# Kernel optimization log

Measured on AMD Instinct MI355X. Metric: run time of the kernel, lower is better.

Reference implementation:

```python
import jax, jax.numpy as jnp
import numpy as np

N, DIM, DK, DV = 8192, 512, 128, 128


def setup_inputs() -> dict:
    key = jax.random.key(0)
    ks = jax.random.split(key, 6)
    s = lambda d: 1.0 / np.sqrt(d)
    return {
        "x": jax.random.normal(ks[0], (N, DIM), jnp.float32),
        "W": jax.random.normal(ks[1], (DK, DIM), jnp.float32) * s(DIM),
        "b": jax.random.normal(ks[2], (DK,), jnp.float32) * s(DIM),
        "Wv": jax.random.normal(ks[3], (DV, DIM), jnp.float32) * s(DIM),
        "bv": jax.random.normal(ks[4], (DV,), jnp.float32) * s(DIM),
        "a": jax.random.normal(ks[5], (2 * DK,), jnp.float32),
    }


def reference(x, W, b, Wv, bv, a):
    dk = a.shape[0] // 2
    wx = x @ W.T + b                      # [n, dk]
    # additive GAT score decomposed into two matvecs + outer sum
    s_src = wx @ a[:dk]                   # [n]
    s_dst = wx @ a[dk:]                   # [n]
    score = s_src[:, None] + s_dst[None, :]  # [n, n]
    score = jax.nn.leaky_relu(score, negative_slope=0.01)
    score = jax.nn.softmax(score, axis=-1)
    v = x @ Wv.T + bv                     # [n, dv]
    return score @ v                      # [n, dv]
```

## Files before the change

### kernel.cpp

```cpp
#include <hip/hip_runtime.h>
#include <math.h>

static constexpr int N    = 8192;
static constexpr int DIM  = 512;
static constexpr int DK   = 128;
static constexpr int DV   = 128;
static constexpr float SLOPE = 0.01f;

static constexpr int NCH  = 512;
static constexpr int CHSZ = 16;
static constexpr int NCOL = 258;

static constexpr int MT  = 128;
static constexpr int BK  = 32;
static constexpr int LDT = 132;

__global__ __launch_bounds__(256) void k_front(const float* __restrict__ x,
                                               const float* __restrict__ W,
                                               const float* __restrict__ b,
                                               const float* __restrict__ a,
                                               float* __restrict__ s_src,
                                               float* __restrict__ s_dst) {
    __shared__ float sa[2 * DK];
    __shared__ float sus[DIM + 32], sud[DIM + 32];
    __shared__ float sc[2];
    int tid = threadIdx.x;
    sa[tid] = a[tid];
    __syncthreads();

    {
        float p = 0.0f;
        if (tid < 64)        p = b[tid] * sa[tid] + b[tid + 64] * sa[tid + 64];
        else if (tid < 128) { int l = tid - 64; p = b[l] * sa[DK + l] + b[l + 64] * sa[DK + 64 + l]; }
#pragma unroll
        for (int off = 32; off > 0; off >>= 1) p += __shfl_down(p, off);
        if (tid == 0)  sc[0] = p;
        if (tid == 64) sc[1] = p;
    }

#pragma unroll
    for (int half = 0; half < 2; ++half) {
        int d = tid + half * 256;
        float us = 0.0f, ud = 0.0f;
#pragma unroll 4
        for (int k = 0; k < DK; ++k) {
            float w = W[(size_t)k * DIM + d];
            us += w * sa[k];
            ud += w * sa[DK + k];
        }
        int dp = d + (d >> 6) * 4;
        sus[dp] = us;
        sud[dp] = ud;
    }
    __syncthreads();

    int r   = tid >> 3;
    int seg = tid & 7;
    int row = blockIdx.x * 32 + r;
    const float* xr = x + (size_t)row * DIM;
    int base  = seg * 64;
    int baseP = base + seg * 4;
    float accs = 0.0f, accd = 0.0f;
#pragma unroll
    for (int i = 0; i < 16; ++i) {
        float4 q  = *reinterpret_cast<const float4*>(xr + base + i * 4);
        float4 u4 = *reinterpret_cast<const float4*>(&sus[baseP + i * 4]);
        float4 w4 = *reinterpret_cast<const float4*>(&sud[baseP + i * 4]);
        accs += q.x * u4.x + q.y * u4.y + q.z * u4.z + q.w * u4.w;
        accd += q.x * w4.x + q.y * w4.y + q.z * w4.z + q.w * w4.w;
    }
#pragma unroll
    for (int off = 4; off > 0; off >>= 1) {
        accs += __shfl_down(accs, off);
        accd += __shfl_down(accd, off);
    }
    if (seg == 0) {
        s_src[row] = accs + sc[0];
        s_dst[row] = accd + sc[1];
    }
}

__global__ __launch_bounds__(256) void k_v(const float* __restrict__ x,
                                           const float* __restrict__ Wv,
                                           float* __restrict__ vpart, int ksplit) {
    __shared__ float At[BK][LDT];
    __shared__ float Bt[BK][LDT];
    int tid = threadIdx.x;
    int mt  = blockIdx.x & 63;
    int ks  = blockIdx.x >> 6;
    int row0 = mt * MT;
    int ksub = DIM / ksplit;
    int kb0  = ks * ksub;
    int nt   = ksub / BK;
    int tx = tid & 15, ty = tid >> 4;

    float acc[8][8];
#pragma unroll
    for (int i = 0; i < 8; ++i)
#pragma unroll
        for (int j = 0; j < 8; ++j) acc[i][j] = 0.0f;

    int fr[4], fk[4];
#pragma unroll
    for (int i = 0; i < 4; ++i) {
        int f = tid + i * 256;
        fr[i] = f >> 3;
        fk[i] = (f & 7) * 4;
    }
    float4 px[4], pw[4];
#pragma unroll
    for (int i = 0; i < 4; ++i) {
        px[i] = *reinterpret_cast<const float4*>(x  + (size_t)(row0 + fr[i]) * DIM + kb0 + fk[i]);
        pw[i] = *reinterpret_cast<const float4*>(Wv + (size_t)fr[i] * DIM + kb0 + fk[i]);
    }

    for (int t = 0; t < nt; ++t) {
#pragma unroll
        for (int i = 0; i < 4; ++i) {
            At[fk[i] + 0][fr[i]] = px[i].x;
            At[fk[i] + 1][fr[i]] = px[i].y;
            At[fk[i] + 2][fr[i]] = px[i].z;
            At[fk[i] + 3][fr[i]] = px[i].w;
            Bt[fk[i] + 0][fr[i]] = pw[i].x;
            Bt[fk[i] + 1][fr[i]] = pw[i].y;
            Bt[fk[i] + 2][fr[i]] = pw[i].z;
            Bt[fk[i] + 3][fr[i]] = pw[i].w;
        }
        __syncthreads();
        if (t < nt - 1) {
            int kb = kb0 + (t + 1) * BK;
#pragma unroll
            for (int i = 0; i < 4; ++i) {
                px[i] = *reinterpret_cast<const float4*>(x  + (size_t)(row0 + fr[i]) * DIM + kb + fk[i]);
                pw[i] = *reinterpret_cast<const float4*>(Wv + (size_t)fr[i] * DIM + kb + fk[i]);
            }
        }
#pragma unroll 4
        for (int kk = 0; kk < BK; ++kk) {
            float4 a0 = *reinterpret_cast<const float4*>(&At[kk][ty * 4]);
            float4 a1 = *reinterpret_cast<const float4*>(&At[kk][64 + ty * 4]);
            float4 b0 = *reinterpret_cast<const float4*>(&Bt[kk][tx * 4]);
            float4 b1 = *reinterpret_cast<const float4*>(&Bt[kk][64 + tx * 4]);
            float av[8] = {a0.x, a0.y, a0.z, a0.w, a1.x, a1.y, a1.z, a1.w};
            float bw[8] = {b0.x, b0.y, b0.z, b0.w, b1.x, b1.y, b1.z, b1.w};
#pragma unroll
            for (int i = 0; i < 8; ++i)
#pragma unroll
                for (int j = 0; j < 8; ++j) acc[i][j] += av[i] * bw[j];
        }
        __syncthreads();
    }

#pragma unroll
    for (int rh = 0; rh < 2; ++rh)
#pragma unroll
        for (int i = 0; i < 4; ++i) {
            int row = row0 + rh * 64 + ty * 4 + i;
            float* dst = vpart + ((size_t)ks * N + row) * DV;
#pragma unroll
            for (int ch = 0; ch < 2; ++ch) {
                float4 o;
                o.x = acc[rh * 4 + i][ch * 4 + 0];
                o.y = acc[rh * 4 + i][ch * 4 + 1];
                o.z = acc[rh * 4 + i][ch * 4 + 2];
                o.w = acc[rh * 4 + i][ch * 4 + 3];
                *reinterpret_cast<float4*>(dst + ch * 64 + tx * 4) = o;
            }
        }
}

__global__ __launch_bounds__(256) void k_rank_scatter(const float* __restrict__ s_dst,
                                                      float* __restrict__ d_sorted,
                                                      int* __restrict__ perm) {
    __shared__ __align__(16) float sd[N];
    __shared__ int part[256];
    int tid = threadIdx.x;
    for (int t = tid; t < N / 4; t += 256)
        reinterpret_cast<float4*>(sd)[t] = reinterpret_cast<const float4*>(s_dst)[t];
    __syncthreads();
    int j0  = blockIdx.x * 16;
    int jj  = tid >> 4;
    int seg = tid & 15;
    int j   = j0 + jj;
    float dj = sd[j];
    int cnt = 0;
    const float4* sdv = reinterpret_cast<const float4*>(sd);
    int cbase = seg * 128;
    for (int c = 0; c < 128; ++c) {
        float4 q = sdv[cbase + c];
        int i0 = (cbase + c) * 4;
        cnt += (q.x < dj || (q.x == dj && (i0 + 0) < j));
        cnt += (q.y < dj || (q.y == dj && (i0 + 1) < j));
        cnt += (q.z < dj || (q.z == dj && (i0 + 2) < j));
        cnt += (q.w < dj || (q.w == dj && (i0 + 3) < j));
    }
    part[tid] = cnt;
    __syncthreads();
    if (tid < 16) {
        int s = 0;
#pragma unroll
        for (int t = 0; t < 16; ++t) s += part[tid * 16 + t];
        int jw = j0 + tid;
        d_sorted[s] = sd[jw];
        perm[s] = jw;
    }
}

__global__ __launch_bounds__(256) void k_vredY(const float* __restrict__ vpart,
                                               const float* __restrict__ bv,
                                               const float* __restrict__ d_sorted,
                                               const int* __restrict__ perm,
                                               float* __restrict__ Y1,
                                               float* __restrict__ Y2,
                                               double* __restrict__ chunk_tot,
                                               int ksplit) {
    __shared__ float sv[CHSZ][DV];
    __shared__ float se1[CHSZ], se2[CHSZ];
    int ch  = blockIdx.x;
    int tid = threadIdx.x;
    int g   = tid >> 5;
    int c4  = tid & 31;
    float dmax = d_sorted[N - 1];
    if (tid < CHSZ) {
        float d = d_sorted[ch * CHSZ + tid];
        se1[tid] = expf(d - dmax);
        se2[tid] = expf(SLOPE * d);
    }
    __syncthreads();
    float4 bb = reinterpret_cast<const float4*>(bv)[c4];
#pragma unroll
    for (int half = 0; half < 2; ++half) {
        int rl = half * 8 + g;
        int r  = ch * CHSZ + rl;
        int j  = perm[r];
        float4 s = {0.f, 0.f, 0.f, 0.f};
        for (int ksp = 0; ksp < ksplit; ++ksp) {
            float4 q = *reinterpret_cast<const float4*>(vpart + ((size_t)ksp * N + j) * DV + c4 * 4);
            s.x += q.x; s.y += q.y; s.z += q.z; s.w += q.w;
        }
        s.x += bb.x; s.y += bb.y; s.z += bb.z; s.w += bb.w;
        *reinterpret_cast<float4*>(&sv[rl][c4 * 4]) = s;
        float e1 = se1[rl], e2 = se2[rl];
        float4 o1 = {e1 * s.x, e1 * s.y, e1 * s.z, e1 * s.w};
        float4 o2 = {e2 * s.x, e2 * s.y, e2 * s.z, e2 * s.w};
        *reinterpret_cast<float4*>(Y1 + (size_t)r * DV + c4 * 4) = o1;
        *reinterpret_cast<float4*>(Y2 + (size_t)r * DV + c4 * 4) = o2;
    }
    __syncthreads();
    int col = tid & 127;
    bool is2 = tid >= 128;
    double acc = 0.0;
#pragma unroll
    for (int k = 0; k < CHSZ; ++k) {
        float e = is2 ? se2[k] : se1[k];
        acc += (double)(e * sv[k][col]);
    }
    chunk_tot[(size_t)ch * NCOL + tid] = acc;
    if (tid == 0) {
        double z = 0.0;
#pragma unroll
        for (int k = 0; k < CHSZ; ++k) z += (double)se1[k];
        chunk_tot[(size_t)ch * NCOL + 256] = z;
    }
    if (tid == 1) {
        double z = 0.0;
#pragma unroll
        for (int k = 0; k < CHSZ; ++k) z += (double)se2[k];
        chunk_tot[(size_t)ch * NCOL + 257] = z;
    }
}

__global__ __launch_bounds__(256) void k_coff(const double* __restrict__ chunk_tot,
                                              double* __restrict__ chunk_off,
                                              double* __restrict__ totals) {
    __shared__ double sp[256];
    int col = blockIdx.x;
    int tid = threadIdx.x;
    double v0 = chunk_tot[(size_t)(2 * tid) * NCOL + col];
    double v1 = chunk_tot[(size_t)(2 * tid + 1) * NCOL + col];
    double p = v0 + v1;
    sp[tid] = p;
    __syncthreads();
    for (int off = 1; off < 256; off <<= 1) {
        double t = (tid >= off) ? sp[tid - off] : 0.0;
        __syncthreads();
        sp[tid] += t;
        __syncthreads();
    }
    double excl = sp[tid] - p;
    chunk_off[(size_t)(2 * tid) * NCOL + col]     = excl;
    chunk_off[(size_t)(2 * tid + 1) * NCOL + col] = excl + v0;
    if (tid == 255) totals[col] = sp[255];
}

__global__ __launch_bounds__(256) void k_scanW(const float* __restrict__ Y1,
                                               const float* __restrict__ Y2,
                                               const float* __restrict__ d_sorted,
                                               const double* __restrict__ chunk_off,
                                               float* __restrict__ P1,
                                               float* __restrict__ P2,
                                               double* __restrict__ pz1,
                                               double* __restrict__ pz2) {
    int ch  = blockIdx.x;
    int tid = threadIdx.x;
    int col = tid & 127;
    bool is2 = tid >= 128;
    const float* Y = is2 ? Y2 : Y1;
    float* P       = is2 ? P2 : P1;
    double acc = chunk_off[(size_t)ch * NCOL + tid];
#pragma unroll
    for (int k = 0; k < CHSZ; ++k) {
        size_t idx = (size_t)(ch * CHSZ + k) * DV + col;
        P[idx] = (float)acc;
        acc += (double)Y[idx];
    }
    if (tid < 2) {
        float dmax = d_sorted[N - 1];
        double z = chunk_off[(size_t)ch * NCOL + 256 + tid];
        double* pz = tid == 0 ? pz1 : pz2;
#pragma unroll
        for (int k = 0; k < CHSZ; ++k) {
            int r = ch * CHSZ + k;
            float d = d_sorted[r];
            float e = (tid == 0) ? expf(d - dmax) : expf(SLOPE * d);
            pz[r] = z;
            z += (double)e;
        }
    }
}

__global__ __launch_bounds__(256) void k_final(const float* __restrict__ s_src,
                                               const float* __restrict__ d_sorted,
                                               const float* __restrict__ P1,
                                               const float* __restrict__ P2,
                                               const double* __restrict__ pz1,
                                               const double* __restrict__ pz2,
                                               const double* __restrict__ totals,
                                               float* __restrict__ out) {
    __shared__ int ski[8];
    __shared__ float ssi[8];
    int tid = threadIdx.x;
    int rbase = blockIdx.x * 8;
    if (tid < 8) {
        int row = rbase + tid;
        float si = s_src[row];
        float thr = -si;
        int lo = 0, hi = N;
        while (lo < hi) {
            int mid = (lo + hi) >> 1;
            if (d_sorted[mid] <= thr) lo = mid + 1; else hi = mid;
        }
        ski[tid] = lo;
        ssi[tid] = si;
    }
    __syncthreads();
    float dmax = d_sorted[N - 1];
    int dv = tid & 127;
    int half = tid >> 7;
    double T1 = totals[dv];
    double T2 = totals[128 + dv];
    double z1T = totals[256], z2T = totals[257];
#pragma unroll
    for (int it = 0; it < 4; ++it) {
        int r2 = it * 2 + half;
        int row = rbase + r2;
        float si = ssi[r2];
        int ki = ski[r2];
        float t = si + dmax;
        float m = t > 0.0f ? t : SLOPE * t;
        float alpha = expf(t - m);
        float beta  = expf(SLOPE * si - m);
        double suf1, sufz1, pre2, prez2;
        if (ki < N) {
            suf1  = T1 - (double)P1[(size_t)ki * DV + dv];
            sufz1 = z1T - pz1[ki];
            pre2  = (double)P2[(size_t)ki * DV + dv];
            prez2 = pz2[ki];
        } else {
            suf1 = 0.0; sufz1 = 0.0; pre2 = T2; prez2 = z2T;
        }
        double num = (double)alpha * suf1  + (double)beta * pre2;
        double den = (double)alpha * sufz1 + (double)beta * prez2;
        out[(size_t)row * DV + dv] = (float)(num / den);
    }
}

extern "C" void kernel_launch(void* const* d_in, const int* in_sizes, int n_in,
                              void* d_out, int out_size, void* d_ws, size_t ws_size,
                              hipStream_t stream) {
    const float* x  = (const float*)d_in[0];
    const float* W  = (const float*)d_in[1];
    const float* b  = (const float*)d_in[2];
    const float* Wv = (const float*)d_in[3];
    const float* bv = (const float*)d_in[4];
    const float* a  = (const float*)d_in[5];
    float* out = (float*)d_out;

    char* base = (char*)d_ws;
    size_t off = 0;
    auto carve = [&](size_t bytes) -> void* {
        void* p = base + off;
        off = (off + bytes + 255) & ~(size_t)255;
        return p;
    };
    float*  s_src     = (float*)carve(N * sizeof(float));
    float*  s_dst     = (float*)carve(N * sizeof(float));
    float*  d_sorted  = (float*)carve(N * sizeof(float));
    int*    perm      = (int*)carve(N * sizeof(int));
    double* pz1       = (double*)carve(N * sizeof(double));
    double* pz2       = (double*)carve(N * sizeof(double));
    double* chunk_tot = (double*)carve((size_t)NCH * NCOL * sizeof(double));
    double* chunk_off = (double*)carve((size_t)NCH * NCOL * sizeof(double));
    double* totals    = (double*)carve(NCOL * sizeof(double));
    float*  Y1        = (float*)carve((size_t)N * DV * sizeof(float));
    float*  Y2        = (float*)carve((size_t)N * DV * sizeof(float));

    const size_t planeB = (size_t)N * DV * sizeof(float);
    size_t avail = ws_size > off ? ws_size - off : 0;
    int ksplit = 2;
    if (avail >= 8 * planeB + 4096)      ksplit = 8;
    else if (avail >= 4 * planeB + 4096) ksplit = 4;
    size_t unionBytes = (size_t)(ksplit > 2 ? ksplit : 2) * planeB;
    char* uni = (char*)carve(unionBytes);
    float* vpart = (float*)uni;
    float* P1    = (float*)uni;
    float* P2    = (float*)(uni + planeB);

    k_front<<<N / 32, 256, 0, stream>>>(x, W, b, a, s_src, s_dst);
    k_v<<<64 * ksplit, 256, 0, stream>>>(x, Wv, vpart, ksplit);
    k_rank_scatter<<<N / 16, 256, 0, stream>>>(s_dst, d_sorted, perm);
    k_vredY<<<NCH, 256, 0, stream>>>(vpart, bv, d_sorted, perm, Y1, Y2, chunk_tot, ksplit);
    k_coff<<<NCOL, 256, 0, stream>>>(chunk_tot, chunk_off, totals);
    k_scanW<<<NCH, 256, 0, stream>>>(Y1, Y2, d_sorted, chunk_off, P1, P2, pz1, pz2);
    k_final<<<N / 8, 256, 0, stream>>>(s_src, d_sorted, P1, P2, pz1, pz2, totals, out);
}
```

Baseline: 169.1 us.

## Fuse front/V GEMM kernels and merge tail stages into one cooperative kernel

Merges the score-projection kernel and the V GEMM into one launch split by block index, with the K-split fixed at 4. The rank, reduction, chunk-offset, scan and final stages become one cooperative kernel separated by grid-wide syncs. Scan results are kept in shared memory across the sync, so the Y1/Y2 round trip through global memory is skipped. This targets launch overhead and inter-kernel gaps. The costs are grid.sync overhead and one block per CU being pinned for the whole tail, with a multi-kernel fallback if the cooperative launch fails.

```diff
diff --git a/kernel.cpp b/kernel.cpp
--- a/kernel.cpp
+++ b/kernel.cpp
@@ -1,5 +1,8 @@
 #include <hip/hip_runtime.h>
+#include <hip/hip_cooperative_groups.h>
 #include <math.h>
+
+namespace cg = cooperative_groups;
 
 static constexpr int N    = 8192;
 static constexpr int DIM  = 512;
@@ -11,174 +14,171 @@
 static constexpr int CHSZ = 16;
 static constexpr int NCOL = 258;
 
+static constexpr int KSPLIT = 4;
+static constexpr int KSUB   = DIM / KSPLIT;
 static constexpr int MT  = 128;
 static constexpr int BK  = 32;
 static constexpr int LDT = 132;
 
-__global__ __launch_bounds__(256) void k_front(const float* __restrict__ x,
-                                               const float* __restrict__ W,
-                                               const float* __restrict__ b,
-                                               const float* __restrict__ a,
-                                               float* __restrict__ s_src,
-                                               float* __restrict__ s_dst) {
+__global__ __launch_bounds__(256) void k_frontv(const float* __restrict__ x,
+                                                const float* __restrict__ W,
+                                                const float* __restrict__ b,
+                                                const float* __restrict__ a,
+                                                const float* __restrict__ Wv,
+                                                float* __restrict__ s_src,
+                                                float* __restrict__ s_dst,
+                                                float* __restrict__ vpart) {
+    __shared__ float At[BK][LDT];
+    __shared__ float Bt[BK][LDT];
     __shared__ float sa[2 * DK];
     __shared__ float sus[DIM + 32], sud[DIM + 32];
     __shared__ float sc[2];
+    int blk = blockIdx.x;
     int tid = threadIdx.x;
-    sa[tid] = a[tid];
-    __syncthreads();
-
-    {
-        float p = 0.0f;
-        if (tid < 64)        p = b[tid] * sa[tid] + b[tid + 64] * sa[tid + 64];
-        else if (tid < 128) { int l = tid - 64; p = b[l] * sa[DK + l] + b[l + 64] * sa[DK + 64 + l]; }
-#pragma unroll
-        for (int off = 32; off > 0; off >>= 1) p += __shfl_down(p, off);
-        if (tid == 0)  sc[0] = p;
-        if (tid == 64) sc[1] = p;
-    }
-
-#pragma unroll
-    for (int half = 0; half < 2; ++half) {
-        int d = tid + half * 256;
-        float us = 0.0f, ud = 0.0f;
+
+    if (blk < 256) {
+        int mt  = blk & 63;
+        int ks  = blk >> 6;
+        int row0 = mt * MT;
+        int kb0  = ks * KSUB;
+        int tx = tid & 15, ty = tid >> 4;
+
+        float acc[8][8];
+#pragma unroll
+        for (int i = 0; i < 8; ++i)
+#pragma unroll
+            for (int j = 0; j < 8; ++j) acc[i][j] = 0.0f;
+
+        int fr[4], fk[4];
+#pragma unroll
+        for (int i = 0; i < 4; ++i) {
+            int f = tid + i * 256;
+            fr[i] = f >> 3;
+            fk[i] = (f & 7) * 4;
+        }
+        float4 px[4], pw[4];
+#pragma unroll
+        for (int i = 0; i < 4; ++i) {
+            px[i] = *reinterpret_cast<const float4*>(x  + (size_t)(row0 + fr[i]) * DIM + kb0 + fk[i]);
+            pw[i] = *reinterpret_cast<const float4*>(Wv + (size_t)fr[i] * DIM + kb0 + fk[i]);
+        }
+        const int nt = KSUB / BK;
+        for (int t = 0; t < nt; ++t) {
+#pragma unroll
+            for (int i = 0; i < 4; ++i) {
+                At[fk[i] + 0][fr[i]] = px[i].x;
+                At[fk[i] + 1][fr[i]] = px[i].y;
+                At[fk[i] + 2][fr[i]] = px[i].z;
+                At[fk[i] + 3][fr[i]] = px[i].w;
+                Bt[fk[i] + 0][fr[i]] = pw[i].x;
+                Bt[fk[i] + 1][fr[i]] = pw[i].y;
+                Bt[fk[i] + 2][fr[i]] = pw[i].z;
+                Bt[fk[i] + 3][fr[i]] = pw[i].w;
+            }
+            __syncthreads();
+            if (t < nt - 1) {
+                int kb = kb0 + (t + 1) * BK;
+#pragma unroll
+                for (int i = 0; i < 4; ++i) {
+                    px[i] = *reinterpret_cast<const float4*>(x  + (size_t)(row0 + fr[i]) * DIM + kb + fk[i]);
+                    pw[i] = *reinterpret_cast<const float4*>(Wv + (size_t)fr[i] * DIM + kb + fk[i]);
+                }
+            }
 #pragma unroll 4
-        for (int k = 0; k < DK; ++k) {
-            float w = W[(size_t)k * DIM + d];
-            us += w * sa[k];
-            ud += w * sa[DK + k];
-        }
-        int dp = d + (d >> 6) * 4;
-        sus[dp] = us;
-        sud[dp] = ud;
-    }
-    __syncthreads();
-
-    int r   = tid >> 3;
-    int seg = tid & 7;
-    int row = blockIdx.x * 32 + r;
-    const float* xr = x + (size_t)row * DIM;
-    int base  = seg * 64;
-    int baseP = base + seg * 4;
-    float accs = 0.0f, accd = 0.0f;
-#pragma unroll
-    for (int i = 0; i < 16; ++i) {
-        float4 q  = *reinterpret_cast<const float4*>(xr + base + i * 4);
-        float4 u4 = *reinterpret_cast<const float4*>(&sus[baseP + i * 4]);
-        float4 w4 = *reinterpret_cast<const float4*>(&sud[baseP + i * 4]);
-        accs += q.x * u4.x + q.y * u4.y + q.z * u4.z + q.w * u4.w;
-        accd += q.x * w4.x + q.y * w4.y + q.z * w4.z + q.w * w4.w;
-    }
-#pragma unroll
-    for (int off = 4; off > 0; off >>= 1) {
-        accs += __shfl_down(accs, off);
-        accd += __shfl_down(accd, off);
-    }
-    if (seg == 0) {
-        s_src[row] = accs + sc[0];
-        s_dst[row] = accd + sc[1];
-    }
-}
-
-__global__ __launch_bounds__(256) void k_v(const float* __restrict__ x,
-                                           const float* __restrict__ Wv,
-                                           float* __restrict__ vpart, int ksplit) {
-    __shared__ float At[BK][LDT];
-    __shared__ float Bt[BK][LDT];
-    int tid = threadIdx.x;
-    int mt  = blockIdx.x & 63;
-    int ks  = blockIdx.x >> 6;
-    int row0 = mt * MT;
-    int ksub = DIM / ksplit;
-    int kb0  = ks * ksub;
-    int nt   = ksub / BK;
-    int tx = tid & 15, ty = tid >> 4;
-
-    float acc[8][8];
-#pragma unroll
-    for (int i = 0; i < 8; ++i)
-#pragma unroll
-        for (int j = 0; j < 8; ++j) acc[i][j] = 0.0f;
-
-    int fr[4], fk[4];
-#pragma unroll
-    for (int i = 0; i < 4; ++i) {
-        int f = tid + i * 256;
-        fr[i] = f >> 3;
-        fk[i] = (f & 7) * 4;
-    }
-    float4 px[4], pw[4];
-#pragma unroll
-    for (int i = 0; i < 4; ++i) {
-        px[i] = *reinterpret_cast<const float4*>(x  + (size_t)(row0 + fr[i]) * DIM + kb0 + fk[i]);
-        pw[i] = *reinterpret_cast<const float4*>(Wv + (size_t)fr[i] * DIM + kb0 + fk[i]);
-    }
-
-    for (int t = 0; t < nt; ++t) {
-#pragma unroll
-        for (int i = 0; i < 4; ++i) {
-            At[fk[i] + 0][fr[i]] = px[i].x;
-            At[fk[i] + 1][fr[i]] = px[i].y;
-            At[fk[i] + 2][fr[i]] = px[i].z;
-            At[fk[i] + 3][fr[i]] = px[i].w;
-            Bt[fk[i] + 0][fr[i]] = pw[i].x;
-            Bt[fk[i] + 1][fr[i]] = pw[i].y;
-            Bt[fk[i] + 2][fr[i]] = pw[i].z;
-            Bt[fk[i] + 3][fr[i]] = pw[i].w;
-        }
+            for (int kk = 0; kk < BK; ++kk) {
+                float4 a0 = *reinterpret_cast<const float4*>(&At[kk][ty * 4]);
+                float4 a1 = *reinterpret_cast<const float4*>(&At[kk][64 + ty * 4]);
+                float4 b0 = *reinterpret_cast<const float4*>(&Bt[kk][tx * 4]);
+                float4 b1 = *reinterpret_cast<const float4*>(&Bt[kk][64 + tx * 4]);
+                float av[8] = {a0.x, a0.y, a0.z, a0.w, a1.x, a1.y, a1.z, a1.w};
+                float bw[8] = {b0.x, b0.y, b0.z, b0.w, b1.x, b1.y, b1.z, b1.w};
+#pragma unroll
+                for (int i = 0; i < 8; ++i)
+#pragma unroll
+                    for (int j = 0; j < 8; ++j) acc[i][j] += av[i] * bw[j];
+            }
+            __syncthreads();
+        }
+#pragma unroll
+        for (int rh = 0; rh < 2; ++rh)
+#pragma unroll
+            for (int i = 0; i < 4; ++i) {
+                int row = row0 + rh * 64 + ty * 4 + i;
+                float* dst = vpart + ((size_t)ks * N + row) * DV;
+#pragma unroll
+                for (int ch = 0; ch < 2; ++ch) {
+                    float4 o;
+                    o.x = acc[rh * 4 + i][ch * 4 + 0];
+                    o.y = acc[rh * 4 + i][ch * 4 + 1];
+                    o.z = acc[rh * 4 + i][ch * 4 + 2];
+                    o.w = acc[rh * 4 + i][ch * 4 + 3];
+                    *reinterpret_cast<float4*>(dst + ch * 64 + tx * 4) = o;
+                }
+            }
+    } else {
+        int fb = blk - 256;
+        sa[tid] = a[tid];
         __syncthreads();
-        if (t < nt - 1) {
-            int kb = kb0 + (t + 1) * BK;
-#pragma unroll
-            for (int i = 0; i < 4; ++i) {
-                px[i] = *reinterpret_cast<const float4*>(x  + (size_t)(row0 + fr[i]) * DIM + kb + fk[i]);
-                pw[i] = *reinterpret_cast<const float4*>(Wv + (size_t)fr[i] * DIM + kb + fk[i]);
+        {
+            float p = 0.0f;
+            if (tid < 64)        p = b[tid] * sa[tid] + b[tid + 64] * sa[tid + 64];
+            else if (tid < 128) { int l = tid - 64; p = b[l] * sa[DK + l] + b[l + 64] * sa[DK + 64 + l]; }
+#pragma unroll
+            for (int off = 32; off > 0; off >>= 1) p += __shfl_down(p, off);
+            if (tid == 0)  sc[0] = p;
+            if (tid == 64) sc[1] = p;
+        }
+#pragma unroll
+        for (int half = 0; half < 2; ++half) {
+            int d = tid + half * 256;
+            float us = 0.0f, ud = 0.0f;
+#pragma unroll 4
+            for (int k = 0; k < DK; ++k) {
+                float w = W[(size_t)k * DIM + d];
+                us += w * sa[k];
+                ud += w * sa[DK + k];
             }
-        }
-#pragma unroll 4
-        for (int kk = 0; kk < BK; ++kk) {
-            float4 a0 = *reinterpret_cast<const float4*>(&At[kk][ty * 4]);
-            float4 a1 = *reinterpret_cast<const float4*>(&At[kk][64 + ty * 4]);
-            float4 b0 = *reinterpret_cast<const float4*>(&Bt[kk][tx * 4]);
-            float4 b1 = *reinterpret_cast<const float4*>(&Bt[kk][64 + tx * 4]);
-            float av[8] = {a0.x, a0.y, a0.z, a0.w, a1.x, a1.y, a1.z, a1.w};
-            float bw[8] = {b0.x, b0.y, b0.z, b0.w, b1.x, b1.y, b1.z, b1.w};
-#pragma unroll
-            for (int i = 0; i < 8; ++i)
-#pragma unroll
-                for (int j = 0; j < 8; ++j) acc[i][j] += av[i] * bw[j];
+            int dp = d + (d >> 6) * 4;
+            sus[dp] = us;
+            sud[dp] = ud;
         }
         __syncthreads();
-    }
-
-#pragma unroll
-    for (int rh = 0; rh < 2; ++rh)
-#pragma unroll
-        for (int i = 0; i < 4; ++i) {
-            int row = row0 + rh * 64 + ty * 4 + i;
-            float* dst = vpart + ((size_t)ks * N + row) * DV;
-#pragma unroll
-            for (int ch = 0; ch < 2; ++ch) {
-                float4 o;
-                o.x = acc[rh * 4 + i][ch * 4 + 0];
-                o.y = acc[rh * 4 + i][ch * 4 + 1];
-                o.z = acc[rh * 4 + i][ch * 4 + 2];
-                o.w = acc[rh * 4 + i][ch * 4 + 3];
-                *reinterpret_cast<float4*>(dst + ch * 64 + tx * 4) = o;
-            }
-        }
-}
-
-__global__ __launch_bounds__(256) void k_rank_scatter(const float* __restrict__ s_dst,
-                                                      float* __restrict__ d_sorted,
-                                                      int* __restrict__ perm) {
-    __shared__ __align__(16) float sd[N];
-    __shared__ int part[256];
-    int tid = threadIdx.x;
+        int r   = tid >> 3;
+        int seg = tid & 7;
+        int row = fb * 32 + r;
+        const float* xr = x + (size_t)row * DIM;
+        int base  = seg * 64;
+        int baseP = base + seg * 4;
+        float accs = 0.0f, accd = 0.0f;
+#pragma unroll
+        for (int i = 0; i < 16; ++i) {
+            float4 q  = *reinterpret_cast<const float4*>(xr + base + i * 4);
+            float4 u4 = *reinterpret_cast<const float4*>(&sus[baseP + i * 4]);
+            float4 w4 = *reinterpret_cast<const float4*>(&sud[baseP + i * 4]);
+            accs += q.x * u4.x + q.y * u4.y + q.z * u4.z + q.w * u4.w;
+            accd += q.x * w4.x + q.y * w4.y + q.z * w4.z + q.w * w4.w;
+        }
+#pragma unroll
+        for (int off = 4; off > 0; off >>= 1) {
+            accs += __shfl_down(accs, off);
+            accd += __shfl_down(accd, off);
+        }
+        if (seg == 0) {
+            s_src[row] = accs + sc[0];
+            s_dst[row] = accd + sc[1];
+        }
+    }
+}
+
+__device__ __forceinline__ void rank_phase(int blk, int tid,
+                                           const float* __restrict__ s_dst,
+                                           float* __restrict__ d_sorted,
+                                           int* __restrict__ perm,
+                                           float* sd, int* part) {
     for (int t = tid; t < N / 4; t += 256)
         reinterpret_cast<float4*>(sd)[t] = reinterpret_cast<const float4*>(s_dst)[t];
     __syncthreads();
-    int j0  = blockIdx.x * 16;
+    int j0  = blk * 16;
     int jj  = tid >> 4;
     int seg = tid & 15;
     int j   = j0 + jj;
@@ -206,20 +206,13 @@
     }
 }
 
-__global__ __launch_bounds__(256) void k_vredY(const float* __restrict__ vpart,
-                                               const float* __restrict__ bv,
-                                               const float* __restrict__ d_sorted,
-                                               const int* __restrict__ perm,
-                                               float* __restrict__ Y1,
-                                               float* __restrict__ Y2,
-                                               double* __restrict__ chunk_tot,
-                                               int ksplit) {
-    __shared__ float sv[CHSZ][DV];
-    __shared__ float se1[CHSZ], se2[CHSZ];
-    int ch  = blockIdx.x;
-    int tid = threadIdx.x;
-    int g   = tid >> 5;
-    int c4  = tid & 31;
+__device__ __forceinline__ void vred_phase(int ch, int tid,
+                                           const float* __restrict__ vpart,
+                                           const float* __restrict__ bv,
+                                           const float* __restrict__ d_sorted,
+                                           const int* __restrict__ perm,
+                                           double* __restrict__ chunk_tot,
+                                           float (*sv)[DV], float* se1, float* se2) {
     float dmax = d_sorted[N - 1];
     if (tid < CHSZ) {
         float d = d_sorted[ch * CHSZ + tid];
@@ -227,6 +220,8 @@
         se2[tid] = expf(SLOPE * d);
     }
     __syncthreads();
+    int g  = tid >> 5;
+    int c4 = tid & 31;
     float4 bb = reinterpret_cast<const float4*>(bv)[c4];
 #pragma unroll
     for (int half = 0; half < 2; ++half) {
@@ -234,17 +229,13 @@
         int r  = ch * CHSZ + rl;
         int j  = perm[r];
         float4 s = {0.f, 0.f, 0.f, 0.f};
-        for (int ksp = 0; ksp < ksplit; ++ksp) {
+#pragma unroll
+        for (int ksp = 0; ksp < KSPLIT; ++ksp) {
             float4 q = *reinterpret_cast<const float4*>(vpart + ((size_t)ksp * N + j) * DV + c4 * 4);
             s.x += q.x; s.y += q.y; s.z += q.z; s.w += q.w;
         }
         s.x += bb.x; s.y += bb.y; s.z += bb.z; s.w += bb.w;
         *reinterpret_cast<float4*>(&sv[rl][c4 * 4]) = s;
-        float e1 = se1[rl], e2 = se2[rl];
-        float4 o1 = {e1 * s.x, e1 * s.y, e1 * s.z, e1 * s.w};
-        float4 o2 = {e2 * s.x, e2 * s.y, e2 * s.z, e2 * s.w};
-        *reinterpret_cast<float4*>(Y1 + (size_t)r * DV + c4 * 4) = o1;
-        *reinterpret_cast<float4*>(Y2 + (size_t)r * DV + c4 * 4) = o2;
     }
     __syncthreads();
     int col = tid & 127;
@@ -270,12 +261,13 @@
     }
 }
 
-__global__ __launch_bounds__(256) void k_coff(const double* __restrict__ chunk_tot,
-                                              double* __restrict__ chunk_off,
-                                              double* __restrict__ totals) {
-    __shared__ double sp[256];
-    int col = blockIdx.x;
-    int tid = threadIdx.x;
+__device__ __forceinline__ void coff_phase(int blk, int tid,
+                                           const double* __restrict__ chunk_tot,
+                                           double* __restrict__ chunk_off,
+                                           double* __restrict__ totals,
+                                           double* sp) {
+    if (blk >= NCOL) return;
+    int col = blk;
     double v0 = chunk_tot[(size_t)(2 * tid) * NCOL + col];
     double v1 = chunk_tot[(size_t)(2 * tid + 1) * NCOL + col];
     double p = v0 + v1;
@@ -293,55 +285,46 @@
     if (tid == 255) totals[col] = sp[255];
 }
 
-__global__ __launch_bounds__(256) void k_scanW(const float* __restrict__ Y1,
-                                               const float* __restrict__ Y2,
-                                               const float* __restrict__ d_sorted,
-                                               const double* __restrict__ chunk_off,
-                                               float* __restrict__ P1,
-                                               float* __restrict__ P2,
-                                               double* __restrict__ pz1,
-                                               double* __restrict__ pz2) {
-    int ch  = blockIdx.x;
-    int tid = threadIdx.x;
+__device__ __forceinline__ void scan_phase(int ch, int tid,
+                                           const double* __restrict__ chunk_off,
+                                           float* __restrict__ P1, float* __restrict__ P2,
+                                           double* __restrict__ pz1, double* __restrict__ pz2,
+                                           const float (*sv)[DV], const float* se1, const float* se2) {
     int col = tid & 127;
     bool is2 = tid >= 128;
-    const float* Y = is2 ? Y2 : Y1;
-    float* P       = is2 ? P2 : P1;
+    const float* se = is2 ? se2 : se1;
+    float* P        = is2 ? P2  : P1;
     double acc = chunk_off[(size_t)ch * NCOL + tid];
 #pragma unroll
     for (int k = 0; k < CHSZ; ++k) {
         size_t idx = (size_t)(ch * CHSZ + k) * DV + col;
         P[idx] = (float)acc;
-        acc += (double)Y[idx];
+        acc += (double)(se[k] * sv[k][col]);
     }
     if (tid < 2) {
-        float dmax = d_sorted[N - 1];
         double z = chunk_off[(size_t)ch * NCOL + 256 + tid];
-        double* pz = tid == 0 ? pz1 : pz2;
+        const float* sez = (tid == 0) ? se1 : se2;
+        double* pz = (tid == 0) ? pz1 : pz2;
 #pragma unroll
         for (int k = 0; k < CHSZ; ++k) {
-            int r = ch * CHSZ + k;
-            float d = d_sorted[r];
-            float e = (tid == 0) ? expf(d - dmax) : expf(SLOPE * d);
-            pz[r] = z;
-            z += (double)e;
-        }
-    }
-}
-
-__global__ __launch_bounds__(256) void k_final(const float* __restrict__ s_src,
-                                               const float* __restrict__ d_sorted,
-                                               const float* __restrict__ P1,
-                                               const float* __restrict__ P2,
-                                               const double* __restrict__ pz1,
-                                               const double* __restrict__ pz2,
-                                               const double* __restrict__ totals,
-                                               float* __restrict__ out) {
-    __shared__ int ski[8];
-    __shared__ float ssi[8];
-    int tid = threadIdx.x;
-    int rbase = blockIdx.x * 8;
-    if (tid < 8) {
+            pz[ch * CHSZ + k] = z;
+            z += (double)sez[k];
+        }
+    }
+}
+
+__device__ __forceinline__ void final_phase(int blk, int tid,
+                                            const float* __restrict__ s_src,
+                                            const float* __restrict__ d_sorted,
+                                            const float* __restrict__ P1,
+                                            const float* __restrict__ P2,
+                                            const double* __restrict__ pz1,
+                                            const double* __restrict__ pz2,
+                                            const double* __restrict__ totals,
+                                            float* __restrict__ out,
+                                            int* ski, float* ssi) {
+    int rbase = blk * 16;
+    if (tid < 16) {
         int row = rbase + tid;
         float si = s_src[row];
         float thr = -si;
@@ -361,7 +344,7 @@
     double T2 = totals[128 + dv];
     double z1T = totals[256], z2T = totals[257];
 #pragma unroll
-    for (int it = 0; it < 4; ++it) {
+    for (int it = 0; it < 8; ++it) {
         int r2 = it * 2 + half;
         int row = rbase + r2;
         float si = ssi[r2];
@@ -383,6 +366,136 @@
         double den = (double)alpha * sufz1 + (double)beta * prez2;
         out[(size_t)row * DV + dv] = (float)(num / den);
     }
+}
+
+__global__ __launch_bounds__(256) void k_tail(const float* __restrict__ vpart,
+                                              const float* __restrict__ bv,
+                                              const float* __restrict__ s_src,
+                                              const float* __restrict__ s_dst,
+                                              float* __restrict__ d_sorted,
+                                              int* __restrict__ perm,
+                                              double* __restrict__ chunk_tot,
+                                              double* __restrict__ chunk_off,
+                                              double* __restrict__ totals,
+                                              float* __restrict__ P1,
+                                              float* __restrict__ P2,
+                                              double* __restrict__ pz1,
+                                              double* __restrict__ pz2,
+                                              float* __restrict__ out) {
+    __shared__ __align__(16) unsigned char smem[33792];
+    float* sd        = (float*)smem;
+    int*   part      = (int*)(smem + 32768);
+    float (*sv)[DV]  = (float(*)[DV])smem;
+    float* se1       = (float*)(smem + 8192);
+    float* se2       = (float*)(smem + 8256);
+    double* sp       = (double*)(smem + 8320);
+    int*   ski       = (int*)(smem + 10368);
+    float* ssi       = (float*)(smem + 10432);
+
+    cg::grid_group grid = cg::this_grid();
+    int blk = blockIdx.x;
+    int tid = threadIdx.x;
+
+    rank_phase(blk, tid, s_dst, d_sorted, perm, sd, part);
+    grid.sync();
+    vred_phase(blk, tid, vpart, bv, d_sorted, perm, chunk_tot, sv, se1, se2);
+    grid.sync();
+    coff_phase(blk, tid, chunk_tot, chunk_off, totals, sp);
+    grid.sync();
+    scan_phase(blk, tid, chunk_off, P1, P2, pz1, pz2, sv, se1, se2);
+    grid.sync();
+    final_phase(blk, tid, s_src, d_sorted, P1, P2, pz1, pz2, totals, out, ski, ssi);
+}
+
+__global__ __launch_bounds__(256) void k_rankS(const float* __restrict__ s_dst,
+                                               float* __restrict__ d_sorted,
+                                               int* __restrict__ perm) {
+    __shared__ __align__(16) float sd[N];
+    __shared__ int part[256];
+    rank_phase(blockIdx.x, threadIdx.x, s_dst, d_sorted, perm, sd, part);
+}
+
+__global__ __launch_bounds__(256) void k_vredYS(const float* __restrict__ vpart,
+                                                const float* __restrict__ bv,
+                                                const float* __restrict__ d_sorted,
+                                                const int* __restrict__ perm,
+                                                float* __restrict__ Y1,
+                                                float* __restrict__ Y2,
+                                                double* __restrict__ chunk_tot) {
+    __shared__ float sv[CHSZ][DV];
+    __shared__ float se1[CHSZ], se2[CHSZ];
+    int ch = blockIdx.x, tid = threadIdx.x;
+    vred_phase(ch, tid, vpart, bv, d_sorted, perm, chunk_tot, sv, se1, se2);
+    __syncthreads();
+    int g  = tid >> 5;
+    int c4 = tid & 31;
+#pragma unroll
+    for (int half = 0; half < 2; ++half) {
+        int rl = half * 8 + g;
+        int r  = ch * CHSZ + rl;
+        float e1 = se1[rl], e2 = se2[rl];
+        float4 s = *reinterpret_cast<const float4*>(&sv[rl][c4 * 4]);
+        float4 o1 = {e1 * s.x, e1 * s.y, e1 * s.z, e1 * s.w};
+        float4 o2 = {e2 * s.x, e2 * s.y, e2 * s.z, e2 * s.w};
+        *reinterpret_cast<float4*>(Y1 + (size_t)r * DV + c4 * 4) = o1;
+        *reinterpret_cast<float4*>(Y2 + (size_t)r * DV + c4 * 4) = o2;
+    }
+}
+
+__global__ __launch_bounds__(256) void k_coffS(const double* __restrict__ chunk_tot,
+                                               double* __restrict__ chunk_off,
+                                               double* __restrict__ totals) {
+    __shared__ double sp[256];
+    coff_phase(blockIdx.x, threadIdx.x, chunk_tot, chunk_off, totals, sp);
+}
+
+__global__ __launch_bounds__(256) void k_scanWS(const float* __restrict__ Y1,
+                                                const float* __restrict__ Y2,
+                                                const float* __restrict__ d_sorted,
+                                                const double* __restrict__ chunk_off,
+                                                float* __restrict__ P1,
+                                                float* __restrict__ P2,
+                                                double* __restrict__ pz1,
+                                                double* __restrict__ pz2) {
+    int ch  = blockIdx.x;
+    int tid = threadIdx.x;
+    int col = tid & 127;
+    bool is2 = tid >= 128;
+    const float* Y = is2 ? Y2 : Y1;
+    float* P       = is2 ? P2 : P1;
+    double acc = chunk_off[(size_t)ch * NCOL + tid];
+#pragma unroll
+    for (int k = 0; k < CHSZ; ++k) {
+        size_t idx = (size_t)(ch * CHSZ + k) * DV + col;
+        P[idx] = (float)acc;
+        acc += (double)Y[idx];
+    }
+    if (tid < 2) {
+        float dmax = d_sorted[N - 1];
+        double z = chunk_off[(size_t)ch * NCOL + 256 + tid];
+        double* pz = tid == 0 ? pz1 : pz2;
+#pragma unroll
+        for (int k = 0; k < CHSZ; ++k) {
+            int r = ch * CHSZ + k;
+            float d = d_sorted[r];
+            float e = (tid == 0) ? expf(d - dmax) : expf(SLOPE * d);
+            pz[r] = z;
+            z += (double)e;
+        }
+    }
+}
+
+__global__ __launch_bounds__(256) void k_finalS(const float* __restrict__ s_src,
+                                                const float* __restrict__ d_sorted,
+                                                const float* __restrict__ P1,
+                                                const float* __restrict__ P2,
+                                                const double* __restrict__ pz1,
+                                                const double* __restrict__ pz2,
+                                                const double* __restrict__ totals,
+                                                float* __restrict__ out) {
+    __shared__ int ski[16];
+    __shared__ float ssi[16];
+    final_phase(blockIdx.x, threadIdx.x, s_src, d_sorted, P1, P2, pz1, pz2, totals, out, ski, ssi);
 }
 
 extern "C" void kernel_launch(void* const* d_in, const int* in_sizes, int n_in,
@@ -416,21 +529,27 @@
     float*  Y2        = (float*)carve((size_t)N * DV * sizeof(float));
 
     const size_t planeB = (size_t)N * DV * sizeof(float);
-    size_t avail = ws_size > off ? ws_size - off : 0;
-    int ksplit = 2;
-    if (avail >= 8 * planeB + 4096)      ksplit = 8;
-    else if (avail >= 4 * planeB + 4096) ksplit = 4;
-    size_t unionBytes = (size_t)(ksplit > 2 ? ksplit : 2) * planeB;
-    char* uni = (char*)carve(unionBytes);
+    char* uni = (char*)carve((size_t)KSPLIT * planeB);
     float* vpart = (float*)uni;
     float* P1    = (float*)uni;
     float* P2    = (float*)(uni + planeB);
 
-    k_front<<<N / 32, 256, 0, stream>>>(x, W, b, a, s_src, s_dst);
-    k_v<<<64 * ksplit, 256, 0, stream>>>(x, Wv, vpart, ksplit);
-    k_rank_scatter<<<N / 16, 256, 0, stream>>>(s_dst, d_sorted, perm);
-    k_vredY<<<NCH, 256, 0, stream>>>(vpart, bv, d_sorted, perm, Y1, Y2, chunk_tot, ksplit);
-    k_coff<<<NCOL, 256, 0, stream>>>(chunk_tot, chunk_off, totals);
-    k_scanW<<<NCH, 256, 0, stream>>>(Y1, Y2, d_sorted, chunk_off, P1, P2, pz1, pz2);
-    k_final<<<N / 8, 256, 0, stream>>>(s_src, d_sorted, P1, P2, pz1, pz2, totals, out);
-}
+    k_frontv<<<512, 256, 0, stream>>>(x, W, b, a, Wv, s_src, s_dst, vpart);
+
+    void* args[] = {
+        (void*)&vpart, (void*)&bv, (void*)&s_src, (void*)&s_dst,
+        (void*)&d_sorted, (void*)&perm, (void*)&chunk_tot, (void*)&chunk_off,
+        (void*)&totals, (void*)&P1, (void*)&P2, (void*)&pz1, (void*)&pz2,
+        (void*)&out
+    };
+    hipError_t err = hipLaunchCooperativeKernel((const void*)k_tail,
+                                                dim3(NCH), dim3(256),
+                                                args, 0, stream);
+    if (err != hipSuccess) {
+        k_rankS<<<NCH, 256, 0, stream>>>(s_dst, d_sorted, perm);
+        k_vredYS<<<NCH, 256, 0, stream>>>(vpart, bv, d_sorted, perm, Y1, Y2, chunk_tot);
+        k_coffS<<<NCOL, 256, 0, stream>>>(chunk_tot, chunk_off, totals);
+        k_scanWS<<<NCH, 256, 0, stream>>>(Y1, Y2, d_sorted, chunk_off, P1, P2, pz1, pz2);
+        k_finalS<<<NCH, 256, 0, stream>>>(s_src, d_sorted, P1, P2, pz1, pz2, totals, out);
+    }
+}
```

Result: slower. 384.0 us (+127.1%).
